# Kernel optimization log

Hardware: AMD Instinct MI355X
Metric: run time of the kernel (lower is better)

## Reference

```python
import jax, jax.numpy as jnp
import numpy as np

B, T, F, H = 32, 2048, 256, 256  # batch, steps, features, n_hidden
FORGET_BIAS = 1.0  # BasicLSTMCell default


def setup_inputs() -> dict:
    key = jax.random.key(0)
    k1, k2, k3, k4, k5 = jax.random.split(key, 5)
    u = lambda k, shape: jax.random.uniform(k, shape, jnp.float32, -0.1, 0.1)
    return {
        "x": jax.random.normal(k1, (B, T, F), jnp.float32),
        "W_fw": u(k2, (F + H, 4 * H)),  # BasicLSTMCell single kernel [in+hidden, 4H]
        "b_fw": jnp.zeros((4 * H,), jnp.float32),
        "W_bw": u(k3, (F + H, 4 * H)),
        "b_bw": jnp.zeros((4 * H,), jnp.float32),
    }


def _lstm_dir(x, W, b):
    # x: [B,T,F]; W: [F+H,4H]; gate order i, j, f, o (BasicLSTMCell)
    Wx, Wh = W[:F], W[F:]
    xg = jnp.einsum('btf,fg->btg', x, Wx) + b  # precompute input contribution [B,T,4H]

    def step(carry, g_t):
        c, h = carry
        gates = g_t + h @ Wh
        i, j, f, o = jnp.split(gates, 4, axis=-1)
        c = c * jax.nn.sigmoid(f + FORGET_BIAS) + jax.nn.sigmoid(i) * jnp.tanh(j)
        h = jnp.tanh(c) * jax.nn.sigmoid(o)
        return (c, h), h

    init = (jnp.zeros((x.shape[0], H), x.dtype), jnp.zeros((x.shape[0], H), x.dtype))
    _, hs = jax.lax.scan(step, init, jnp.swapaxes(xg, 0, 1))  # [T,B,H]
    return jnp.swapaxes(hs, 0, 1)  # [B,T,H]


def reference(x, W_fw, b_fw, W_bw, b_bw):
    out_fw = _lstm_dir(x, W_fw, b_fw)
    out_bw = _lstm_dir(x[:, ::-1], W_bw, b_bw)[:, ::-1]  # backward direction
    return jnp.concatenate([out_fw, out_bw], axis=-1)  # [B,T,2H]
```

## Files before the change

kernel.cpp:

```cpp
#include <hip/hip_runtime.h>

#define T_LEN 2048

typedef _Float16 f16x8 __attribute__((ext_vector_type(8)));
typedef float f32x4 __attribute__((ext_vector_type(4)));
typedef unsigned int u32;

__device__ __forceinline__ float sigm(float v) { return 1.f / (1.f + __expf(-v)); }

__device__ __forceinline__ void* swzA(_Float16* base, int row, int k) {
  int byte = row * 1024 + k * 2;
  byte ^= (row & 7) << 4;
  return (void*)((char*)base + byte);
}

__global__ __launch_bounds__(1024, 4) void bilstm_kernel(
    const float* __restrict__ x, const float* __restrict__ Wfw,
    const float* __restrict__ bfw, const float* __restrict__ Wbw,
    const float* __restrict__ bbw, float* __restrict__ out,
    u32* __restrict__ hglob) {
  const int g = blockIdx.x & 3;
  const int m = blockIdx.x >> 2;
  const int dir = g >> 1, bh = g & 1;
  const int tid = threadIdx.x;
  const int w = tid >> 6;
  const int lane = tid & 63;
  const int l15 = lane & 15, l4 = lane >> 4;

  const float* W = dir ? Wbw : Wfw;
  const float* bias = dir ? bbw : bfw;

  __shared__ _Float16 Alds[16 * 512];
  __shared__ float Glds[16 * 260];

  const int p = w >> 2;
  const int cbase = p * 64 + (w & 3) * 16;
  const int gcol = p * 256 + 64 * m + (w & 3) * 16 + l15;
  f16x8 wB[16];
#pragma unroll
  for (int kk = 0; kk < 16; ++kk) {
    const int kb = kk * 32 + l4 * 8;
    f16x8 h;
#pragma unroll
    for (int j = 0; j < 8; ++j) h[j] = (_Float16)W[(kb + j) * 1024 + gcol];
    wB[kk] = h;
  }
  const float bcol = bias[gcol] + ((p == 2) ? 1.f : 0.f);

  const int cs = tid >> 6;
  const int cd = tid & 63;
  float c = 0.f;

  u32* Hg = hglob + g * (2 * 16 * 256);
  const int pd1 = 64 * ((m + 1) & 3) + cd;
  const int pd2 = 64 * ((m + 2) & 3) + cd;
  const int pd3 = 64 * ((m + 3) & 3) + cd;
  u32* mypub[2] = {Hg + (0 * 16 + cs) * 256 + 64 * m + cd,
                   Hg + (1 * 16 + cs) * 256 + 64 * m + cd};

  {
    uint2 z = {0u, 0u};
    *(uint2*)swzA(Alds, cs, 256 + 4 * cd) = z;
  }
  const int tx0 = dir ? (T_LEN - 1) : 0;
  f32x4 xv = *(const f32x4*)(x + (((bh * 16 + cs) * T_LEN + tx0) << 8) + 4 * cd);

  for (int t = 0; t < T_LEN; ++t) {
    const int tx = dir ? (T_LEN - 1 - t) : t;

    {
      union { _Float16 h[4]; uint2 q; } ux;
#pragma unroll
      for (int j = 0; j < 4; ++j) ux.h[j] = (_Float16)xv[j];
      *(uint2*)swzA(Alds, cs, 4 * cd) = ux.q;
    }
    __syncthreads();

    const u32 want = (u32)t;
    const u32* Hp = Hg + (((t & 1) ^ 1) * 16 + cs) * 256;
    u32 s1 = 0, s2 = 0, s3 = 0;
    if (t > 0) {
      s1 = __hip_atomic_load(Hp + pd1, __ATOMIC_RELAXED, __HIP_MEMORY_SCOPE_AGENT);
      s2 = __hip_atomic_load(Hp + pd2, __ATOMIC_RELAXED, __HIP_MEMORY_SCOPE_AGENT);
      s3 = __hip_atomic_load(Hp + pd3, __ATOMIC_RELAXED, __HIP_MEMORY_SCOPE_AGENT);
    }

    {
      const int tn = (t + 1 < T_LEN) ? t + 1 : t;
      const int txn = dir ? (T_LEN - 1 - tn) : tn;
      xv = *(const f32x4*)(x + (((bh * 16 + cs) * T_LEN + txn) << 8) + 4 * cd);
    }

    f32x4 acc = {bcol, bcol, bcol, bcol};
#pragma unroll
    for (int kk = 0; kk < 8; ++kk) {
      f16x8 a = *(const f16x8*)swzA(Alds, l15, kk * 32 + l4 * 8);
      acc = __builtin_amdgcn_mfma_f32_16x16x32_f16(a, wB[kk], acc, 0, 0, 0);
    }

    if (t > 0) {
      while ((s1 >> 16) != want || (s2 >> 16) != want || (s3 >> 16) != want) {
        s1 = __hip_atomic_load(Hp + pd1, __ATOMIC_RELAXED, __HIP_MEMORY_SCOPE_AGENT);
        s2 = __hip_atomic_load(Hp + pd2, __ATOMIC_RELAXED, __HIP_MEMORY_SCOPE_AGENT);
        s3 = __hip_atomic_load(Hp + pd3, __ATOMIC_RELAXED, __HIP_MEMORY_SCOPE_AGENT);
      }
      *(unsigned short*)swzA(Alds, cs, 256 + pd1) = (unsigned short)(s1 & 0xffffu);
      *(unsigned short*)swzA(Alds, cs, 256 + pd2) = (unsigned short)(s2 & 0xffffu);
      *(unsigned short*)swzA(Alds, cs, 256 + pd3) = (unsigned short)(s3 & 0xffffu);
    }
    __syncthreads();

#pragma unroll
    for (int kk = 8; kk < 16; ++kk) {
      f16x8 a = *(const f16x8*)swzA(Alds, l15, kk * 32 + l4 * 8);
      acc = __builtin_amdgcn_mfma_f32_16x16x32_f16(a, wB[kk], acc, 0, 0, 0);
    }

    {
      float* gw = Glds + cbase + l15;
      const int r = l4 * 4;
#pragma unroll
      for (int v = 0; v < 4; ++v) gw[(r + v) * 260] = acc[v];
    }
    __syncthreads();

    const float* Gp = Glds + cs * 260 + cd;
    const float gi = Gp[0 * 64], gj = Gp[1 * 64], gf = Gp[2 * 64], go = Gp[3 * 64];
    c = c * sigm(gf) + sigm(gi) * (2.f * sigm(gj + gj) - 1.f);
    const float h = (2.f * sigm(c + c) - 1.f) * sigm(go);

    union { _Float16 hf; unsigned short us; } cv;
    cv.hf = (_Float16)h;
    __hip_atomic_store(mypub[t & 1], (((u32)(t + 1)) << 16) | (u32)cv.us,
                       __ATOMIC_RELAXED, __HIP_MEMORY_SCOPE_AGENT);
    *(unsigned short*)swzA(Alds, cs, 256 + 64 * m + cd) = cv.us;
    __builtin_nontemporal_store(
        h, out + (((bh * 16 + cs) * T_LEN + tx) << 9) + dir * 256 + 64 * m + cd);
  }
}

extern "C" void kernel_launch(void* const* d_in, const int* in_sizes, int n_in,
                              void* d_out, int out_size, void* d_ws,
                              size_t ws_size, hipStream_t stream) {
  const float* x = (const float*)d_in[0];
  const float* Wfw = (const float*)d_in[1];
  const float* bfw = (const float*)d_in[2];
  const float* Wbw = (const float*)d_in[3];
  const float* bbw = (const float*)d_in[4];
  float* out = (float*)d_out;

  u32* hglob = (u32*)d_ws;
  (void)hipMemsetAsync(hglob, 0, 4 * 2 * 16 * 256 * sizeof(u32), stream);

  bilstm_kernel<<<dim3(16), dim3(1024), 0, stream>>>(x, Wfw, bfw, Wbw, bbw, out,
                                                     hglob);
}
```

Before: 4.826 ms.

## Poll peer hidden state via sc0 loads, reorder own-slice MFMAs, remap blocks to XCD

Launches 32 blocks and exits half of them, so each group of four cooperating blocks uses bid&7 for its group id. This appears to place the group on the same XCD so that L2-coherent sc0 loads are enough for exchanging hidden state. Peer h values are now polled with inline-asm sc0 global loads, which avoid the agent-scope atomic path. After 24 failed tries the poll falls back to atomic loads. The block's own h-slice MFMAs, whose inputs are already in LDS, are moved before the spin-wait to overlap work with synchronisation. The approach depends on an undocumented block-to-XCD mapping and on sc0 load coherence, so correctness relies on that fallback if the placement assumption fails.

```diff
diff --git a/kernel.cpp b/kernel.cpp
--- a/kernel.cpp
+++ b/kernel.cpp
@@ -14,13 +14,30 @@
   return (void*)((char*)base + byte);
 }
 
+__device__ __forceinline__ void issue3_sc0(const u32* p1, const u32* p2,
+                                           const u32* p3, u32& a, u32& b,
+                                           u32& c) {
+  asm volatile(
+      "global_load_dword %0, %3, off sc0\n\t"
+      "global_load_dword %1, %4, off sc0\n\t"
+      "global_load_dword %2, %5, off sc0"
+      : "=&v"(a), "=&v"(b), "=&v"(c)
+      : "v"(p1), "v"(p2), "v"(p3)
+      : "memory");
+}
+__device__ __forceinline__ void wait3(u32& a, u32& b, u32& c) {
+  asm volatile("s_waitcnt vmcnt(0)" : "+v"(a), "+v"(b), "+v"(c)::"memory");
+}
+
 __global__ __launch_bounds__(1024, 4) void bilstm_kernel(
     const float* __restrict__ x, const float* __restrict__ Wfw,
     const float* __restrict__ bfw, const float* __restrict__ Wbw,
     const float* __restrict__ bbw, float* __restrict__ out,
     u32* __restrict__ hglob) {
-  const int g = blockIdx.x & 3;
-  const int m = blockIdx.x >> 2;
+  const int bid = blockIdx.x;
+  if ((bid & 7) >= 4) return;
+  const int g = bid & 7;
+  const int m = bid >> 3;
   const int dir = g >> 1, bh = g & 1;
   const int tid = threadIdx.x;
   const int w = tid >> 6;
@@ -50,13 +67,14 @@
   const int cs = tid >> 6;
   const int cd = tid & 63;
   float c = 0.f;
+  bool use_mall = false;
 
   u32* Hg = hglob + g * (2 * 16 * 256);
   const int pd1 = 64 * ((m + 1) & 3) + cd;
   const int pd2 = 64 * ((m + 2) & 3) + cd;
   const int pd3 = 64 * ((m + 3) & 3) + cd;
-  u32* mypub[2] = {Hg + (0 * 16 + cs) * 256 + 64 * m + cd,
-                   Hg + (1 * 16 + cs) * 256 + 64 * m + cd};
+  u32* my0 = Hg + (0 * 16 + cs) * 256 + 64 * m + cd;
+  u32* my1 = Hg + (1 * 16 + cs) * 256 + 64 * m + cd;
 
   {
     uint2 z = {0u, 0u};
@@ -77,13 +95,9 @@
     __syncthreads();
 
     const u32 want = (u32)t;
-    const u32* Hp = Hg + (((t & 1) ^ 1) * 16 + cs) * 256;
+    u32* Hp = Hg + (((t & 1) ^ 1) * 16 + cs) * 256;
     u32 s1 = 0, s2 = 0, s3 = 0;
-    if (t > 0) {
-      s1 = __hip_atomic_load(Hp + pd1, __ATOMIC_RELAXED, __HIP_MEMORY_SCOPE_AGENT);
-      s2 = __hip_atomic_load(Hp + pd2, __ATOMIC_RELAXED, __HIP_MEMORY_SCOPE_AGENT);
-      s3 = __hip_atomic_load(Hp + pd3, __ATOMIC_RELAXED, __HIP_MEMORY_SCOPE_AGENT);
-    }
+    if (t > 0) issue3_sc0(Hp + pd1, Hp + pd2, Hp + pd3, s1, s2, s3);
 
     {
       const int tn = (t + 1 < T_LEN) ? t + 1 : t;
@@ -97,12 +111,29 @@
       f16x8 a = *(const f16x8*)swzA(Alds, l15, kk * 32 + l4 * 8);
       acc = __builtin_amdgcn_mfma_f32_16x16x32_f16(a, wB[kk], acc, 0, 0, 0);
     }
+#pragma unroll
+    for (int q = 0; q < 4; ++q) {
+      if (q == m) {
+        f16x8 a0 = *(const f16x8*)swzA(Alds, l15, (8 + 2 * q) * 32 + l4 * 8);
+        acc = __builtin_amdgcn_mfma_f32_16x16x32_f16(a0, wB[8 + 2 * q], acc, 0, 0, 0);
+        f16x8 a1 = *(const f16x8*)swzA(Alds, l15, (9 + 2 * q) * 32 + l4 * 8);
+        acc = __builtin_amdgcn_mfma_f32_16x16x32_f16(a1, wB[9 + 2 * q], acc, 0, 0, 0);
+      }
+    }
 
     if (t > 0) {
+      wait3(s1, s2, s3);
+      int tries = 0;
       while ((s1 >> 16) != want || (s2 >> 16) != want || (s3 >> 16) != want) {
-        s1 = __hip_atomic_load(Hp + pd1, __ATOMIC_RELAXED, __HIP_MEMORY_SCOPE_AGENT);
-        s2 = __hip_atomic_load(Hp + pd2, __ATOMIC_RELAXED, __HIP_MEMORY_SCOPE_AGENT);
-        s3 = __hip_atomic_load(Hp + pd3, __ATOMIC_RELAXED, __HIP_MEMORY_SCOPE_AGENT);
+        if (use_mall) {
+          s1 = __hip_atomic_load(Hp + pd1, __ATOMIC_RELAXED, __HIP_MEMORY_SCOPE_AGENT);
+          s2 = __hip_atomic_load(Hp + pd2, __ATOMIC_RELAXED, __HIP_MEMORY_SCOPE_AGENT);
+          s3 = __hip_atomic_load(Hp + pd3, __ATOMIC_RELAXED, __HIP_MEMORY_SCOPE_AGENT);
+        } else {
+          issue3_sc0(Hp + pd1, Hp + pd2, Hp + pd3, s1, s2, s3);
+          wait3(s1, s2, s3);
+          if (++tries > 24) use_mall = true;
+        }
       }
       *(unsigned short*)swzA(Alds, cs, 256 + pd1) = (unsigned short)(s1 & 0xffffu);
       *(unsigned short*)swzA(Alds, cs, 256 + pd2) = (unsigned short)(s2 & 0xffffu);
@@ -111,9 +142,13 @@
     __syncthreads();
 
 #pragma unroll
-    for (int kk = 8; kk < 16; ++kk) {
-      f16x8 a = *(const f16x8*)swzA(Alds, l15, kk * 32 + l4 * 8);
-      acc = __builtin_amdgcn_mfma_f32_16x16x32_f16(a, wB[kk], acc, 0, 0, 0);
+    for (int q = 0; q < 4; ++q) {
+      if (q != m) {
+        f16x8 a0 = *(const f16x8*)swzA(Alds, l15, (8 + 2 * q) * 32 + l4 * 8);
+        acc = __builtin_amdgcn_mfma_f32_16x16x32_f16(a0, wB[8 + 2 * q], acc, 0, 0, 0);
+        f16x8 a1 = *(const f16x8*)swzA(Alds, l15, (9 + 2 * q) * 32 + l4 * 8);
+        acc = __builtin_amdgcn_mfma_f32_16x16x32_f16(a1, wB[9 + 2 * q], acc, 0, 0, 0);
+      }
     }
 
     {
@@ -131,7 +166,8 @@
 
     union { _Float16 hf; unsigned short us; } cv;
     cv.hf = (_Float16)h;
-    __hip_atomic_store(mypub[t & 1], (((u32)(t + 1)) << 16) | (u32)cv.us,
+    u32* pub = (t & 1) ? my1 : my0;
+    __hip_atomic_store(pub, (((u32)(t + 1)) << 16) | (u32)cv.us,
                        __ATOMIC_RELAXED, __HIP_MEMORY_SCOPE_AGENT);
     *(unsigned short*)swzA(Alds, cs, 256 + 64 * m + cd) = cv.us;
     __builtin_nontemporal_store(
@@ -152,6 +188,6 @@
   u32* hglob = (u32*)d_ws;
   (void)hipMemsetAsync(hglob, 0, 4 * 2 * 16 * 256 * sizeof(u32), stream);
 
-  bilstm_kernel<<<dim3(16), dim3(1024), 0, stream>>>(x, Wfw, bfw, Wbw, bbw, out,
+  bilstm_kernel<<<dim3(32), dim3(1024), 0, stream>>>(x, Wfw, bfw, Wbw, bbw, out,
                                                      hglob);
 }
```

After: 4.916 ms. Within noise of the previous version (+1.9%).

## Hoist input projection into chunked GEMM and run recurrence per single workgroup

Applied to the files above, without the earlier changes.

The input projection x·Wx leaves the recurrent loop and becomes a separate parallel MFMA GEMM, computed in time chunks into an fp16 workspace. The recurrence now runs one 1024-thread workgroup per direction/batch-half holding the full Wh. Most of Wh lives in registers, part in LDS, and one k-slice is streamed from a packed global buffer each step. This removes the cross-workgroup atomic spin synchronization of the earlier 16-block design and the per-step x loads and conversions. In exchange only 4 workgroups do the serial work, each doing four times the MFMA work per step, and the gate inputs are rounded to fp16.

```diff
diff --git a/kernel.cpp b/kernel.cpp
--- a/kernel.cpp
+++ b/kernel.cpp
@@ -5,137 +5,224 @@
 typedef _Float16 f16x8 __attribute__((ext_vector_type(8)));
 typedef float f32x4 __attribute__((ext_vector_type(4)));
 typedef unsigned int u32;
+typedef unsigned short u16;
 
 __device__ __forceinline__ float sigm(float v) { return 1.f / (1.f + __expf(-v)); }
 
-__device__ __forceinline__ void* swzA(_Float16* base, int row, int k) {
-  int byte = row * 1024 + k * 2;
-  byte ^= (row & 7) << 4;
-  return (void*)((char*)base + byte);
-}
-
-__global__ __launch_bounds__(1024, 4) void bilstm_kernel(
+__global__ __launch_bounds__(256) void wh_pack(const float* __restrict__ Wfw,
+                                               const float* __restrict__ Wbw,
+                                               u16* __restrict__ whk5) {
+  const int s = blockIdx.x * 256 + threadIdx.x;
+  const int dir = s >> 12, r = s & 4095;
+  const int blk = r >> 6, lane = r & 63;
+  const int p = blk >> 4, w = blk & 15;
+  const int l15 = lane & 15, l4 = lane >> 4;
+  const float* W = dir ? Wbw : Wfw;
+  const int col = p * 256 + 16 * w + l15;
+  union { _Float16 h[8]; uint4 q; } u;
+#pragma unroll
+  for (int j = 0; j < 8; ++j)
+    u.h[j] = (_Float16)W[(size_t)(256 + 160 + 8 * l4 + j) * 1024 + col];
+  *(uint4*)(whk5 + ((size_t)dir * 4096 + (size_t)blk * 64 + lane) * 8) = u.q;
+}
+
+__global__ __launch_bounds__(256) void xg_gemm(
     const float* __restrict__ x, const float* __restrict__ Wfw,
     const float* __restrict__ bfw, const float* __restrict__ Wbw,
-    const float* __restrict__ bbw, float* __restrict__ out,
-    u32* __restrict__ hglob) {
-  const int g = blockIdx.x & 3;
-  const int m = blockIdx.x >> 2;
+    const float* __restrict__ bbw, u16* __restrict__ xg, int t0, int chunkT) {
+  const int dir = blockIdx.z;
+  const int mrow0 = blockIdx.x * 64;
+  const int ncol0 = blockIdx.y * 64;
+  const float* W = dir ? Wbw : Wfw;
+  const float* bias = dir ? bbw : bfw;
+  const int tid = threadIdx.x;
+  const int w = tid >> 6, lane = tid & 63, l15 = lane & 15, l4 = lane >> 4;
+
+  __shared__ _Float16 At[64 * 32];
+  __shared__ _Float16 Bt[64 * 32];
+
+  const int b = mrow0 / chunkT;
+  const int sbase = mrow0 % chunkT;
+
+  f32x4 acc[4] = {{0,0,0,0},{0,0,0,0},{0,0,0,0},{0,0,0,0}};
+  const int ar = tid >> 2, acq = tid & 3;
+  const int bc = tid >> 2, bkq = tid & 3;
+
+  for (int kk0 = 0; kk0 < 256; kk0 += 32) {
+    {
+      const int sloc = sbase + ar;
+      const int tx = dir ? (T_LEN - 1 - (t0 + sloc)) : (t0 + sloc);
+      const float* xr = x + ((size_t)b * T_LEN + tx) * 256 + kk0 + 8 * acq;
+      f32x4 v0 = *(const f32x4*)xr;
+      f32x4 v1 = *(const f32x4*)(xr + 4);
+      union { _Float16 h[8]; uint4 q; } u;
+#pragma unroll
+      for (int j = 0; j < 4; ++j) { u.h[j] = (_Float16)v0[j]; u.h[4 + j] = (_Float16)v1[j]; }
+      int byte = ar * 64 + 16 * acq;  byte ^= (ar & 3) << 4;
+      *(uint4*)((char*)At + byte) = u.q;
+    }
+    {
+      const float* wc = W + (size_t)(kk0 + 8 * bkq) * 1024 + ncol0 + bc;
+      union { _Float16 h[8]; uint4 q; } u;
+#pragma unroll
+      for (int j = 0; j < 8; ++j) u.h[j] = (_Float16)wc[(size_t)j * 1024];
+      int byte = bc * 64 + 16 * bkq;  byte ^= (bc & 3) << 4;
+      *(uint4*)((char*)Bt + byte) = u.q;
+    }
+    __syncthreads();
+    f16x8 bfrag;
+    {
+      const int col = w * 16 + l15;
+      int byte = col * 64 + 16 * l4;  byte ^= (col & 3) << 4;
+      bfrag = *(const f16x8*)((char*)Bt + byte);
+    }
+#pragma unroll
+    for (int mt = 0; mt < 4; ++mt) {
+      const int row = mt * 16 + l15;
+      int byte = row * 64 + 16 * l4;  byte ^= (row & 3) << 4;
+      f16x8 afrag = *(const f16x8*)((char*)At + byte);
+      acc[mt] = __builtin_amdgcn_mfma_f32_16x16x32_f16(afrag, bfrag, acc[mt], 0, 0, 0);
+    }
+    __syncthreads();
+  }
+  const int gcol = ncol0 + w * 16 + l15;
+  const int pp = gcol >> 8, dd = gcol & 255;
+  const float badd = bias[gcol] + ((pp == 2) ? 1.f : 0.f);
+#pragma unroll
+  for (int mt = 0; mt < 4; ++mt) {
+#pragma unroll
+    for (int v = 0; v < 4; ++v) {
+      const int sloc = sbase + mt * 16 + 4 * l4 + v;
+      union { _Float16 hf; u16 us; } cv;
+      cv.hf = (_Float16)(acc[mt][v] + badd);
+      xg[((size_t)(dir * 32 + b) * chunkT + sloc) * 1024 + dd * 4 + pp] = cv.us;
+    }
+  }
+}
+
+__global__ __launch_bounds__(1024) void rnn_chunk(
+    const u16* __restrict__ xg, const float* __restrict__ Wfw,
+    const float* __restrict__ Wbw, const u16* __restrict__ whk5,
+    float* __restrict__ out, float* __restrict__ state_c,
+    u16* __restrict__ state_h, int t0, int t1, int chunkT) {
+  const int g = blockIdx.x;
   const int dir = g >> 1, bh = g & 1;
   const int tid = threadIdx.x;
-  const int w = tid >> 6;
-  const int lane = tid & 63;
-  const int l15 = lane & 15, l4 = lane >> 4;
-
+  const int w = tid >> 6, lane = tid & 63, l15 = lane & 15, l4 = lane >> 4;
   const float* W = dir ? Wbw : Wfw;
-  const float* bias = dir ? bbw : bfw;
-
-  __shared__ _Float16 Alds[16 * 512];
-  __shared__ float Glds[16 * 260];
-
-  const int p = w >> 2;
-  const int cbase = p * 64 + (w & 3) * 16;
-  const int gcol = p * 256 + 64 * m + (w & 3) * 16 + l15;
-  f16x8 wB[16];
-#pragma unroll
-  for (int kk = 0; kk < 16; ++kk) {
-    const int kb = kk * 32 + l4 * 8;
-    f16x8 h;
-#pragma unroll
-    for (int j = 0; j < 8; ++j) h[j] = (_Float16)W[(kb + j) * 1024 + gcol];
-    wB[kk] = h;
-  }
-  const float bcol = bias[gcol] + ((p == 2) ? 1.f : 0.f);
-
-  const int cs = tid >> 6;
-  const int cd = tid & 63;
-  float c = 0.f;
-
-  u32* Hg = hglob + g * (2 * 16 * 256);
-  const int pd1 = 64 * ((m + 1) & 3) + cd;
-  const int pd2 = 64 * ((m + 2) & 3) + cd;
-  const int pd3 = 64 * ((m + 3) & 3) + cd;
-  u32* mypub[2] = {Hg + (0 * 16 + cs) * 256 + 64 * m + cd,
-                   Hg + (1 * 16 + cs) * 256 + 64 * m + cd};
-
+
+  __shared__ u16 WL[2 * 4 * 16 * 64 * 8];
+  __shared__ _Float16 H[2][16 * 256];
+
+  f16x8 wB[5][4];
+#pragma unroll
+  for (int kt = 0; kt < 5; ++kt)
+#pragma unroll
+    for (int p = 0; p < 4; ++p) {
+      const int col = p * 256 + 16 * w + l15;
+      f16x8 h;
+#pragma unroll
+      for (int j = 0; j < 8; ++j)
+        h[j] = (_Float16)W[(size_t)(256 + kt * 32 + l4 * 8 + j) * 1024 + col];
+      wB[kt][p] = h;
+    }
+#pragma unroll
+  for (int kt2 = 0; kt2 < 2; ++kt2)
+#pragma unroll
+    for (int p = 0; p < 4; ++p) {
+      const int col = p * 256 + 16 * w + l15;
+      union { _Float16 h[8]; uint4 q; } u;
+#pragma unroll
+      for (int j = 0; j < 8; ++j)
+        u.h[j] = (_Float16)W[(size_t)(256 + 192 + kt2 * 32 + l4 * 8 + j) * 1024 + col];
+      *(uint4*)&WL[(((kt2 * 4 + p) * 16 + w) * 64 + lane) * 8] = u.q;
+    }
+
+  const int d = 16 * w + l15;
+  float c[4];
   {
-    uint2 z = {0u, 0u};
-    *(uint2*)swzA(Alds, cs, 256 + 4 * cd) = z;
-  }
-  const int tx0 = dir ? (T_LEN - 1) : 0;
-  f32x4 xv = *(const f32x4*)(x + (((bh * 16 + cs) * T_LEN + tx0) << 8) + 4 * cd);
-
-  for (int t = 0; t < T_LEN; ++t) {
-    const int tx = dir ? (T_LEN - 1 - t) : t;
-
-    {
-      union { _Float16 h[4]; uint2 q; } ux;
-#pragma unroll
-      for (int j = 0; j < 4; ++j) ux.h[j] = (_Float16)xv[j];
-      *(uint2*)swzA(Alds, cs, 4 * cd) = ux.q;
+#pragma unroll
+    for (int v = 0; v < 4; ++v) {
+      const int seq = 4 * l4 + v;
+      const int sidx = (dir * 32 + bh * 16 + seq) * 256 + d;
+      u16 hb;
+      if (t0 == 0) { c[v] = 0.f; hb = 0; }
+      else { c[v] = state_c[sidx]; hb = state_h[sidx]; }
+      int byte = seq * 512 + d * 2;  byte ^= (seq & 7) << 4;
+      *(u16*)((char*)H[0] + byte) = hb;
+    }
+  }
+  __syncthreads();
+
+  const u16* wk5 = whk5 + ((size_t)dir * 4096 + (size_t)w * 64 + lane) * 8;
+  const size_t xgrow0 = (size_t)(dir * 32 + bh * 16 + 4 * l4) * chunkT;
+
+  for (int s = t0; s < t1; ++s) {
+    const int cur = (s - t0) & 1;
+    const _Float16* Hc = H[cur];
+
+    f16x8 k5[4];
+#pragma unroll
+    for (int p = 0; p < 4; ++p)
+      k5[p] = *(const f16x8*)(wk5 + (size_t)p * (16 * 64 * 8));
+    ushort4 xv[4];
+#pragma unroll
+    for (int v = 0; v < 4; ++v)
+      xv[v] = *(const ushort4*)(xg + ((xgrow0 + (size_t)v * chunkT) + (s - t0)) * 1024 + d * 4);
+
+    f32x4 acc[4] = {{0,0,0,0},{0,0,0,0},{0,0,0,0},{0,0,0,0}};
+#pragma unroll
+    for (int kt = 0; kt < 5; ++kt) {
+      int byte = l15 * 512 + (kt * 32 + l4 * 8) * 2;  byte ^= (l15 & 7) << 4;
+      f16x8 a = *(const f16x8*)((const char*)Hc + byte);
+#pragma unroll
+      for (int p = 0; p < 4; ++p)
+        acc[p] = __builtin_amdgcn_mfma_f32_16x16x32_f16(a, wB[kt][p], acc[p], 0, 0, 0);
+    }
+#pragma unroll
+    for (int kt2 = 0; kt2 < 2; ++kt2) {
+      int byte = l15 * 512 + ((6 + kt2) * 32 + l4 * 8) * 2;  byte ^= (l15 & 7) << 4;
+      f16x8 a = *(const f16x8*)((const char*)Hc + byte);
+#pragma unroll
+      for (int p = 0; p < 4; ++p) {
+        f16x8 bb = *(const f16x8*)&WL[(((kt2 * 4 + p) * 16 + w) * 64 + lane) * 8];
+        acc[p] = __builtin_amdgcn_mfma_f32_16x16x32_f16(a, bb, acc[p], 0, 0, 0);
+      }
+    }
+    {
+      int byte = l15 * 512 + (5 * 32 + l4 * 8) * 2;  byte ^= (l15 & 7) << 4;
+      f16x8 a = *(const f16x8*)((const char*)Hc + byte);
+#pragma unroll
+      for (int p = 0; p < 4; ++p)
+        acc[p] = __builtin_amdgcn_mfma_f32_16x16x32_f16(a, k5[p], acc[p], 0, 0, 0);
+    }
+
+    const int tx = dir ? (T_LEN - 1 - s) : s;
+#pragma unroll
+    for (int v = 0; v < 4; ++v) {
+      const int seq = 4 * l4 + v;
+      const float gi = acc[0][v] + (float)*(const _Float16*)&xv[v].x;
+      const float gj = acc[1][v] + (float)*(const _Float16*)&xv[v].y;
+      const float gf = acc[2][v] + (float)*(const _Float16*)&xv[v].z;
+      const float go = acc[3][v] + (float)*(const _Float16*)&xv[v].w;
+      c[v] = c[v] * sigm(gf) + sigm(gi) * (2.f * sigm(gj + gj) - 1.f);
+      const float h = (2.f * sigm(c[v] + c[v]) - 1.f) * sigm(go);
+      union { _Float16 hf; u16 us; } cv;
+      cv.hf = (_Float16)h;
+      int byte = seq * 512 + d * 2;  byte ^= (seq & 7) << 4;
+      *(u16*)((char*)H[cur ^ 1] + byte) = cv.us;
+      __builtin_nontemporal_store(
+          h, out + ((size_t)(bh * 16 + seq) * T_LEN + tx) * 512 + dir * 256 + d);
     }
     __syncthreads();
-
-    const u32 want = (u32)t;
-    const u32* Hp = Hg + (((t & 1) ^ 1) * 16 + cs) * 256;
-    u32 s1 = 0, s2 = 0, s3 = 0;
-    if (t > 0) {
-      s1 = __hip_atomic_load(Hp + pd1, __ATOMIC_RELAXED, __HIP_MEMORY_SCOPE_AGENT);
-      s2 = __hip_atomic_load(Hp + pd2, __ATOMIC_RELAXED, __HIP_MEMORY_SCOPE_AGENT);
-      s3 = __hip_atomic_load(Hp + pd3, __ATOMIC_RELAXED, __HIP_MEMORY_SCOPE_AGENT);
-    }
-
-    {
-      const int tn = (t + 1 < T_LEN) ? t + 1 : t;
-      const int txn = dir ? (T_LEN - 1 - tn) : tn;
-      xv = *(const f32x4*)(x + (((bh * 16 + cs) * T_LEN + txn) << 8) + 4 * cd);
-    }
-
-    f32x4 acc = {bcol, bcol, bcol, bcol};
-#pragma unroll
-    for (int kk = 0; kk < 8; ++kk) {
-      f16x8 a = *(const f16x8*)swzA(Alds, l15, kk * 32 + l4 * 8);
-      acc = __builtin_amdgcn_mfma_f32_16x16x32_f16(a, wB[kk], acc, 0, 0, 0);
-    }
-
-    if (t > 0) {
-      while ((s1 >> 16) != want || (s2 >> 16) != want || (s3 >> 16) != want) {
-        s1 = __hip_atomic_load(Hp + pd1, __ATOMIC_RELAXED, __HIP_MEMORY_SCOPE_AGENT);
-        s2 = __hip_atomic_load(Hp + pd2, __ATOMIC_RELAXED, __HIP_MEMORY_SCOPE_AGENT);
-        s3 = __hip_atomic_load(Hp + pd3, __ATOMIC_RELAXED, __HIP_MEMORY_SCOPE_AGENT);
-      }
-      *(unsigned short*)swzA(Alds, cs, 256 + pd1) = (unsigned short)(s1 & 0xffffu);
-      *(unsigned short*)swzA(Alds, cs, 256 + pd2) = (unsigned short)(s2 & 0xffffu);
-      *(unsigned short*)swzA(Alds, cs, 256 + pd3) = (unsigned short)(s3 & 0xffffu);
-    }
-    __syncthreads();
-
-#pragma unroll
-    for (int kk = 8; kk < 16; ++kk) {
-      f16x8 a = *(const f16x8*)swzA(Alds, l15, kk * 32 + l4 * 8);
-      acc = __builtin_amdgcn_mfma_f32_16x16x32_f16(a, wB[kk], acc, 0, 0, 0);
-    }
-
-    {
-      float* gw = Glds + cbase + l15;
-      const int r = l4 * 4;
-#pragma unroll
-      for (int v = 0; v < 4; ++v) gw[(r + v) * 260] = acc[v];
-    }
-    __syncthreads();
-
-    const float* Gp = Glds + cs * 260 + cd;
-    const float gi = Gp[0 * 64], gj = Gp[1 * 64], gf = Gp[2 * 64], go = Gp[3 * 64];
-    c = c * sigm(gf) + sigm(gi) * (2.f * sigm(gj + gj) - 1.f);
-    const float h = (2.f * sigm(c + c) - 1.f) * sigm(go);
-
-    union { _Float16 hf; unsigned short us; } cv;
-    cv.hf = (_Float16)h;
-    __hip_atomic_store(mypub[t & 1], (((u32)(t + 1)) << 16) | (u32)cv.us,
-                       __ATOMIC_RELAXED, __HIP_MEMORY_SCOPE_AGENT);
-    *(unsigned short*)swzA(Alds, cs, 256 + 64 * m + cd) = cv.us;
-    __builtin_nontemporal_store(
-        h, out + (((bh * 16 + cs) * T_LEN + tx) << 9) + dir * 256 + 64 * m + cd);
+  }
+#pragma unroll
+  for (int v = 0; v < 4; ++v) {
+    const int seq = 4 * l4 + v;
+    const int sidx = (dir * 32 + bh * 16 + seq) * 256 + d;
+    state_c[sidx] = c[v];
+    int byte = seq * 512 + d * 2;  byte ^= (seq & 7) << 4;
+    state_h[sidx] = *(const u16*)((const char*)H[(t1 - t0) & 1] + byte);
   }
 }
 
@@ -149,9 +236,20 @@
   const float* bbw = (const float*)d_in[4];
   float* out = (float*)d_out;
 
-  u32* hglob = (u32*)d_ws;
-  (void)hipMemsetAsync(hglob, 0, 4 * 2 * 16 * 256 * sizeof(u32), stream);
-
-  bilstm_kernel<<<dim3(16), dim3(1024), 0, stream>>>(x, Wfw, bfw, Wbw, bbw, out,
-                                                     hglob);
-}
+  float* state_c = (float*)d_ws;
+  u16* state_h = (u16*)((char*)d_ws + 64 * 1024);
+  u16* whk5 = (u16*)((char*)d_ws + 128 * 1024);
+  u16* xg = (u16*)((char*)d_ws + (1 << 20));
+
+  int chunkT = 1024;
+  while (chunkT > 64 && (size_t)131072 * chunkT + (1 << 20) > ws_size)
+    chunkT >>= 1;
+
+  wh_pack<<<dim3(32), dim3(256), 0, stream>>>(Wfw, Wbw, whk5);
+  for (int t0 = 0; t0 < T_LEN; t0 += chunkT) {
+    xg_gemm<<<dim3((32 * chunkT) / 64, 16, 2), dim3(256), 0, stream>>>(
+        x, Wfw, bfw, Wbw, bbw, xg, t0, chunkT);
+    rnn_chunk<<<dim3(4), dim3(1024), 0, stream>>>(
+        xg, Wfw, Wbw, whk5, out, state_c, state_h, t0, t0 + chunkT, chunkT);
+  }
+}
```

Measured after the change: 12.95 ms. 168% more time.
